# Kernel tuning notes

Hardware: AMD Instinct MI355X
Metric: run time of the kernel (lower is better)

The kernel has to match this reference:

```python
import jax, jax.numpy as jnp
import numpy as np

N = 50000
E = 1600000

def setup_inputs() -> dict:
    key = jax.random.key(0)
    ks = jax.random.split(key, 8)
    x = jax.random.normal(ks[0], (N, 512), dtype=jnp.float32)
    edge_index = jax.random.randint(ks[1], (2, E), 0, N, dtype=jnp.int32).astype(jnp.int64)
    eigenvectors = jax.random.normal(ks[2], (N, 128), dtype=jnp.float32)
    W1 = jax.random.normal(ks[3], (512, 128), dtype=jnp.float32) * 0.04
    b1 = jnp.zeros((128,), dtype=jnp.float32)
    W2 = jax.random.normal(ks[4], (128, 64), dtype=jnp.float32) * 0.09
    b2 = jnp.zeros((64,), dtype=jnp.float32)
    lin_W = jax.random.normal(ks[5], (128, 64), dtype=jnp.float32) * 0.09
    W3 = jax.random.normal(ks[6], (128, 40), dtype=jnp.float32) * 0.09
    b3 = jnp.zeros((40,), dtype=jnp.float32)
    return {"x": x, "edge_index": edge_index, "eigenvectors": eigenvectors,
            "W1": W1, "b1": b1, "W2": W2, "b2": b2, "lin_W": lin_W, "W3": W3, "b3": b3}

def _gcn_norm(edge_index, num_nodes):
    # add self loops, then symmetric normalization D^-1/2 (A+I) D^-1/2
    loop = jnp.arange(num_nodes, dtype=edge_index.dtype)
    row = jnp.concatenate([edge_index[0], loop])  # source
    col = jnp.concatenate([edge_index[1], loop])  # target
    w = jnp.ones(row.shape[0], dtype=jnp.float32)
    deg = jax.ops.segment_sum(w, col, num_segments=num_nodes)
    dis = jnp.where(deg > 0, 1.0 / jnp.sqrt(deg), 0.0)
    norm = dis[row] * dis[col]  # [E+N]
    return row, col, norm

def _gcn_conv(h, W, b, row, col, norm, num_nodes):
    h = h @ W                                  # [N, d_out] linear first (PyG order)
    msg = h[row] * norm[:, None]               # gather + scale, [E+N, d_out]
    out = jax.ops.segment_sum(msg, col, num_segments=num_nodes)  # scatter-add
    return out + b

def reference(x, edge_index, eigenvectors, W1, b1, W2, b2, lin_W, W3, b3):
    num_nodes = x.shape[0]
    row, col, norm = _gcn_norm(edge_index, num_nodes)
    h = jax.nn.relu(_gcn_conv(x, W1, b1, row, col, norm, num_nodes))
    # dropout omitted: eval mode (deterministic reference)
    h = jax.nn.relu(_gcn_conv(h, W2, b2, row, col, norm, num_nodes))
    xp = eigenvectors @ lin_W                  # Linear(spec_in, spec_out, bias=False)
    h = jnp.concatenate([h, xp], axis=1)       # [N, h2+spec_out]
    h = _gcn_conv(h, W3, b3, row, col, norm, num_nodes)
    return jax.nn.log_softmax(h, axis=1)
```

## Files before the change

### kernel.cpp

```cpp
#include <hip/hip_runtime.h>
#include <cstdint>
#include <cstddef>

constexpr int BLK = 256;
constexpr int NB = 128;

static inline size_t ws_align(size_t x) { return (x + 255) & ~size_t(255); }

typedef __attribute__((ext_vector_type(8))) short bf16x8;
typedef __attribute__((ext_vector_type(4))) float f32x4;

__device__ inline unsigned short f2bf(float f) {
  unsigned int u = __float_as_uint(f);
  unsigned int r = (u + 0x7fffu + ((u >> 16) & 1u)) >> 16;
  return (unsigned short)r;
}
__device__ inline float bf2f(unsigned short u) {
  return __uint_as_float(((unsigned int)u) << 16);
}
__device__ inline float bf2f_lo(unsigned int w) {
  return __uint_as_float(w << 16);
}
__device__ inline float bf2f_hi(unsigned int w) {
  return __uint_as_float(w & 0xffff0000u);
}

__device__ inline void gload16(const void* gp, void* lp) {
  __builtin_amdgcn_global_load_lds(
      (const __attribute__((address_space(1))) void*)gp,
      (__attribute__((address_space(3))) void*)lp, 16, 0, 0);
}

__global__ void k_pack_wt(const int* __restrict__ ei, unsigned int* __restrict__ pk,
                          int* __restrict__ cnt, int E, int nChunk,
                          const float* __restrict__ W1, const float* __restrict__ W2,
                          const float* __restrict__ linW, const float* __restrict__ W3,
                          unsigned short* __restrict__ WT1, unsigned short* __restrict__ WT2,
                          unsigned short* __restrict__ WTl, unsigned short* __restrict__ WT3) {
  if (blockIdx.x >= NB) {
    int i = (blockIdx.x - NB) * BLK + threadIdx.x;
    if (i < 65536) {
      int n = i >> 9, k = i & 511;
      WT1[i] = f2bf(W1[(size_t)k * 128 + n]);
    } else if (i < 73728) {
      int j = i - 65536; int n = j >> 7, k = j & 127;
      WT2[j] = f2bf(W2[(size_t)k * 64 + n]);
    } else if (i < 81920) {
      int j = i - 73728; int n = j >> 7, k = j & 127;
      WTl[j] = f2bf(linW[(size_t)k * 64 + n]);
    } else if (i < 88064) {
      int j = i - 81920; int n = j >> 7, k = j & 127;
      WT3[j] = f2bf(n < 40 ? W3[(size_t)k * 40 + n] : 0.f);
    }
    return;
  }
  __shared__ int hist[256];
  for (int t = threadIdx.x; t < 256; t += BLK) hist[t] = 0;
  __syncthreads();
  int allz = 1;
  #pragma unroll 8
  for (int i = 0; i < 32; ++i) allz &= (ei[2 * i + 1] == 0) ? 1 : 0;
  const bool i64 = allz != 0;
  int beg = blockIdx.x * nChunk, end = min(beg + nChunk, E);
  for (int i = beg + threadIdx.x; i < end; i += BLK) {
    int row, col;
    if (i64) { row = ei[2 * i]; col = ei[2 * (E + i)]; }
    else     { row = ei[i];     col = ei[E + i]; }
    unsigned int p = ((unsigned int)col << 16) | (unsigned int)row;
    pk[i] = p;
    atomicAdd(&hist[col >> 8], 1);
  }
  __syncthreads();
  for (int t = threadIdx.x; t < 256; t += BLK) cnt[blockIdx.x * 256 + t] = hist[t];
}

__global__ void k_wscan(const int* __restrict__ cnt, int* __restrict__ woffs,
                        int* __restrict__ base, int nb, int E) {
  __shared__ int wsums[5];
  int w = threadIdx.x;
  int s = 0;
  for (int b = 0; b < nb; ++b) s += cnt[b * 256 + w];
  int lane = w & 63, wv = w >> 6;
  int x = s;
  #pragma unroll
  for (int sh = 1; sh < 64; sh <<= 1) { int t = __shfl_up(x, sh); if (lane >= sh) x += t; }
  if (lane == 63) wsums[wv] = x;
  __syncthreads();
  if (w == 0) { int a = 0; for (int k = 0; k < 4; ++k) { int t = wsums[k]; wsums[k] = a; a += t; } }
  __syncthreads();
  int excl = x - s + wsums[wv];
  woffs[w] = excl;
  if (w == 255) woffs[256] = excl + s;
  int start = excl;
  for (int b = 0; b < nb; ++b) { base[b * 256 + w] = start; start += cnt[b * 256 + w]; }
}

__global__ void k_part_scatter(const unsigned int* __restrict__ pk,
                               const int* __restrict__ base,
                               unsigned int* __restrict__ P, int E, int nChunk) {
  __shared__ int cur[256];
  for (int t = threadIdx.x; t < 256; t += BLK) cur[t] = base[blockIdx.x * 256 + t];
  __syncthreads();
  int beg = blockIdx.x * nChunk, end = min(beg + nChunk, E);
  for (int i = beg + threadIdx.x; i < end; i += BLK) {
    unsigned int p = pk[i];
    int pos = atomicAdd(&cur[p >> 24], 1);
    P[pos] = p;
  }
}

__global__ void k_window_build(const unsigned int* __restrict__ P,
                               const int* __restrict__ woffs,
                               float* __restrict__ dis, int* __restrict__ offs,
                               int* __restrict__ csr, int N, int E) {
  __shared__ int hist[256];
  __shared__ int wsums[5];
  __shared__ int lbase[256];
  const int node0 = blockIdx.x * 256;
  const int t = threadIdx.x;
  hist[t] = 0;
  __syncthreads();
  const int beg = woffs[blockIdx.x], end = woffs[blockIdx.x + 1];
  for (int i = beg + t; i < end; i += BLK)
    atomicAdd(&hist[(P[i] >> 16) & 255], 1);
  __syncthreads();
  const int dg = hist[t];
  if (node0 + t < N) dis[node0 + t] = 1.0f / sqrtf((float)(dg + 1));
  int lane = t & 63, wv = t >> 6;
  int x = dg;
  #pragma unroll
  for (int sh = 1; sh < 64; sh <<= 1) { int q = __shfl_up(x, sh); if (lane >= sh) x += q; }
  if (lane == 63) wsums[wv] = x;
  __syncthreads();
  if (t == 0) { int a = 0; for (int k = 0; k < 4; ++k) { int q = wsums[k]; wsums[k] = a; a += q; } }
  __syncthreads();
  const int goff = beg + (x - dg + wsums[wv]);
  if (node0 + t < N) offs[node0 + t] = goff;
  lbase[t] = goff;
  __syncthreads();
  for (int i = beg + t; i < end; i += BLK) {
    unsigned int p = P[i];
    int pos = atomicAdd(&lbase[(p >> 16) & 255], 1);
    csr[pos] = (int)(p & 0xffffu);
  }
  if (blockIdx.x == 0 && t == 0) offs[N] = E;
}

__global__ __launch_bounds__(256)
void k_gemm1(const float* __restrict__ x, const unsigned short* __restrict__ WT,
             const float* __restrict__ dis, unsigned short* __restrict__ C, int N) {
  __shared__ float As[2][128 * 32];
  __shared__ unsigned short Wsl[2][4 * 128 * 8];
  const int tid = threadIdx.x;
  const int lane = tid & 63, wv = tid >> 6;
  const int m = lane & 15, kq = lane >> 4;
  const int row0 = blockIdx.x * 128;

  const int r8 = lane >> 3;
  const int c8 = lane & 7;
  int agrow[4];
  #pragma unroll
  for (int jj = 0; jj < 4; ++jj) {
    int gr = row0 + wv * 32 + jj * 8 + r8;
    agrow[jj] = gr < N ? gr : N - 1;
  }

  f32x4 acc[2][8];
  #pragma unroll
  for (int mr = 0; mr < 2; ++mr)
    #pragma unroll
    for (int t = 0; t < 8; ++t) acc[mr][t] = {0.f, 0.f, 0.f, 0.f};

  auto STAGE = [&](int pb, int kb) {
    #pragma unroll
    for (int jj = 0; jj < 4; ++jj) {
      const float* src = x + (size_t)agrow[jj] * 512 + kb * 32 + (c8 ^ r8) * 4;
      gload16(src, &As[pb][(wv * 32 + jj * 8) * 32]);
    }
    #pragma unroll
    for (int jj = 0; jj < 2; ++jj) {
      int issue = wv * 2 + jj;
      int slot = issue >> 1, half = issue & 1;
      const unsigned short* src = WT + (size_t)(half * 64 + lane) * 512 + kb * 32 + slot * 8;
      gload16(src, &Wsl[pb][slot * 1024 + half * 512]);
    }
  };

  STAGE(0, 0);
  __syncthreads();

  #pragma unroll 1
  for (int t = 0; t < 16; ++t) {
    const int p = t & 1;
    if (t < 15) STAGE(p ^ 1, t + 1);

    const char* Ab = (const char*)As[p];
    const char* Wb = (const char*)Wsl[p];
    bf16x8 af[2];
    #pragma unroll
    for (int mr = 0; mr < 2; ++mr) {
      int row = wv * 32 + mr * 16 + m;
      int s = row & 7;
      f32x4 lo = *(const f32x4*)(Ab + row * 128 + ((kq * 2) ^ s) * 16);
      f32x4 hi = *(const f32x4*)(Ab + row * 128 + ((kq * 2 + 1) ^ s) * 16);
      af[mr][0] = (short)f2bf(lo[0]); af[mr][1] = (short)f2bf(lo[1]);
      af[mr][2] = (short)f2bf(lo[2]); af[mr][3] = (short)f2bf(lo[3]);
      af[mr][4] = (short)f2bf(hi[0]); af[mr][5] = (short)f2bf(hi[1]);
      af[mr][6] = (short)f2bf(hi[2]); af[mr][7] = (short)f2bf(hi[3]);
    }
    #pragma unroll
    for (int tt = 0; tt < 8; ++tt) {
      bf16x8 bf = *(const bf16x8*)(Wb + kq * 2048 + (tt * 16 + m) * 16);
      #pragma unroll
      for (int mr = 0; mr < 2; ++mr)
        acc[mr][tt] = __builtin_amdgcn_mfma_f32_16x16x32_bf16(af[mr], bf, acc[mr][tt], 0, 0, 0);
    }
    __syncthreads();
  }

  #pragma unroll
  for (int mr = 0; mr < 2; ++mr)
    #pragma unroll
    for (int r = 0; r < 4; ++r) {
      int rr = row0 + wv * 32 + mr * 16 + kq * 4 + r;
      if (rr < N) {
        float s = dis[rr];
        #pragma unroll
        for (int t = 0; t < 8; ++t)
          C[(size_t)rr * 128 + t * 16 + m] = f2bf(acc[mr][t][r] * s);
      }
    }
}

template<int NT, int MR, bool AF32>
__device__ inline void mgemm_body(int bi, const void* __restrict__ Av,
                                  const unsigned short* __restrict__ WT,
                                  const float* __restrict__ dis, unsigned short* __restrict__ C,
                                  int ldc, int NOUT, int N) {
  constexpr int K = 128;
  const int tid = threadIdx.x;
  const int lane = tid & 63;
  const int wv = tid >> 6;
  const int m = lane & 15;
  const int kq = lane >> 4;
  const int orow = bi * (64 * MR) + wv * (16 * MR);

  int rowc[MR];
  #pragma unroll
  for (int mr = 0; mr < MR; ++mr) {
    int row = orow + mr * 16 + m;
    rowc[mr] = row < N ? row : N - 1;
  }

  f32x4 acc[MR][NT];
  #pragma unroll
  for (int mr = 0; mr < MR; ++mr)
    #pragma unroll
    for (int t = 0; t < NT; ++t) acc[mr][t] = {0.f, 0.f, 0.f, 0.f};

  #pragma unroll 4
  for (int k0 = 0; k0 < K; k0 += 32) {
    bf16x8 af[MR];
    #pragma unroll
    for (int mr = 0; mr < MR; ++mr) {
      if constexpr (AF32) {
        const float* Arow = (const float*)Av + (size_t)rowc[mr] * K + kq * 8 + k0;
        float4 a0 = *(const float4*)Arow;
        float4 a1 = *(const float4*)(Arow + 4);
        af[mr][0] = (short)f2bf(a0.x); af[mr][1] = (short)f2bf(a0.y);
        af[mr][2] = (short)f2bf(a0.z); af[mr][3] = (short)f2bf(a0.w);
        af[mr][4] = (short)f2bf(a1.x); af[mr][5] = (short)f2bf(a1.y);
        af[mr][6] = (short)f2bf(a1.z); af[mr][7] = (short)f2bf(a1.w);
      } else {
        const unsigned short* Arow = (const unsigned short*)Av + (size_t)rowc[mr] * K + kq * 8 + k0;
        af[mr] = *(const bf16x8*)Arow;
      }
    }
    bf16x8 bf[NT];
    #pragma unroll
    for (int t = 0; t < NT; ++t)
      bf[t] = *(const bf16x8*)(WT + (size_t)(t * 16 + m) * K + k0 + kq * 8);
    #pragma unroll
    for (int t = 0; t < NT; ++t)
      #pragma unroll
      for (int mr = 0; mr < MR; ++mr)
        acc[mr][t] = __builtin_amdgcn_mfma_f32_16x16x32_bf16(af[mr], bf[t], acc[mr][t], 0, 0, 0);
  }
  #pragma unroll
  for (int mr = 0; mr < MR; ++mr) {
    #pragma unroll
    for (int r = 0; r < 4; ++r) {
      int rr = orow + mr * 16 + kq * 4 + r;
      if (rr < N) {
        float s = dis ? dis[rr] : 1.f;
        #pragma unroll
        for (int t = 0; t < NT; ++t) {
          int cc = t * 16 + m;
          if (cc < NOUT)
            C[(size_t)rr * ldc + cc] = f2bf(acc[mr][t][r] * s);
        }
      }
    }
  }
}

__global__ __launch_bounds__(256)
void k_mgemm2x(const unsigned short* __restrict__ G, const unsigned short* __restrict__ WT2,
               const float* __restrict__ dis, unsigned short* __restrict__ F,
               const float* __restrict__ eig, const unsigned short* __restrict__ WTl,
               unsigned short* __restrict__ XP, int N, int nA) {
  if ((int)blockIdx.x < nA)
    mgemm_body<4, 2, false>(blockIdx.x, G, WT2, dis, F, 64, 64, N);
  else
    mgemm_body<4, 2, true>(blockIdx.x - nA, eig, WTl, nullptr, XP, 64, 64, N);
}

__global__ __launch_bounds__(256)
void k_mgemm3(const unsigned short* __restrict__ H2, const unsigned short* __restrict__ XP,
              const unsigned short* __restrict__ WT3, const float* __restrict__ dis,
              unsigned short* __restrict__ C, int N) {
  constexpr int NT = 3, MR = 2;
  const int tid = threadIdx.x;
  const int lane = tid & 63;
  const int wv = tid >> 6;
  const int m = lane & 15;
  const int kq = lane >> 4;
  const int orow = blockIdx.x * (64 * MR) + wv * (16 * MR);

  int rowc[MR];
  #pragma unroll
  for (int mr = 0; mr < MR; ++mr) {
    int row = orow + mr * 16 + m;
    rowc[mr] = row < N ? row : N - 1;
  }

  f32x4 acc[MR][NT];
  #pragma unroll
  for (int mr = 0; mr < MR; ++mr)
    #pragma unroll
    for (int t = 0; t < NT; ++t) acc[mr][t] = {0.f, 0.f, 0.f, 0.f};

  #pragma unroll 4
  for (int k0 = 0; k0 < 128; k0 += 32) {
    const unsigned short* Abase = (k0 < 64) ? H2 : XP;
    const int kk = (k0 & 63) + kq * 8;
    bf16x8 af[MR];
    #pragma unroll
    for (int mr = 0; mr < MR; ++mr)
      af[mr] = *(const bf16x8*)(Abase + (size_t)rowc[mr] * 64 + kk);
    bf16x8 bf[NT];
    #pragma unroll
    for (int t = 0; t < NT; ++t)
      bf[t] = *(const bf16x8*)(WT3 + (size_t)(t * 16 + m) * 128 + k0 + kq * 8);
    #pragma unroll
    for (int t = 0; t < NT; ++t)
      #pragma unroll
      for (int mr = 0; mr < MR; ++mr)
        acc[mr][t] = __builtin_amdgcn_mfma_f32_16x16x32_bf16(af[mr], bf[t], acc[mr][t], 0, 0, 0);
  }
  #pragma unroll
  for (int mr = 0; mr < MR; ++mr) {
    #pragma unroll
    for (int r = 0; r < 4; ++r) {
      int rr = orow + mr * 16 + kq * 4 + r;
      if (rr < N) {
        float s = dis[rr];
        #pragma unroll
        for (int t = 0; t < NT; ++t) {
          int cc = t * 16 + m;
          if (cc < 40)
            C[(size_t)rr * 40 + cc] = f2bf(acc[mr][t][r] * s);
        }
      }
    }
  }
}

template<int D, bool RELU>
__launch_bounds__(BLK)
__global__ void k_agg2(const unsigned short* __restrict__ g, int ldg,
                       const float* __restrict__ dis, const float* __restrict__ bias,
                       const int* __restrict__ offs, const int* __restrict__ csr,
                       unsigned short* __restrict__ dst, int ldd, int N) {
  constexpr int CPL = D / 32;
  int wid = (blockIdx.x * BLK + threadIdx.x) >> 6;
  int lane = threadIdx.x & 63;
  if (wid >= N) return;
  const int l5 = lane >> 5, c = lane & 31;
  float acc[CPL];
  #pragma unroll
  for (int k = 0; k < CPL; ++k) acc[k] = 0.f;

  auto addrow = [&](int r) {
    if constexpr (CPL == 4) {
      uint2 w = *(const uint2*)&g[(size_t)r * ldg + c * 4];
      acc[0] += bf2f_lo(w.x); acc[1] += bf2f_hi(w.x);
      acc[2] += bf2f_lo(w.y); acc[3] += bf2f_hi(w.y);
    } else {
      unsigned int w = *(const unsigned int*)&g[(size_t)r * ldg + c * 2];
      acc[0] += bf2f_lo(w); acc[1] += bf2f_hi(w);
    }
  };

  if (l5 == 0) addrow(wid);
  int beg = offs[wid], end = offs[wid + 1];
  for (int e0 = beg; e0 < end; e0 += 64) {
    int cnt = end - e0; if (cnt > 64) cnt = 64;
    int u = (lane < cnt) ? csr[e0 + lane] : 0;
    int j = 0;
    for (; j + 3 < cnt; j += 4) {
      int r0 = __shfl(u, j + l5);
      int r1 = __shfl(u, j + 2 + l5);
      addrow(r0); addrow(r1);
    }
    for (; j < cnt; j += 2) {
      int jj = j + l5;
      int r0 = __shfl(u, jj < cnt ? jj : j);
      if (jj < cnt) addrow(r0);
    }
  }
  #pragma unroll
  for (int k = 0; k < CPL; ++k) acc[k] += __shfl_xor(acc[k], 32);

  if (l5 == 0) {
    float dv = dis[wid];
    float o[CPL];
    #pragma unroll
    for (int k = 0; k < CPL; ++k) {
      o[k] = dv * acc[k] + bias[c * CPL + k];
      if constexpr (RELU) o[k] = fmaxf(o[k], 0.f);
    }
    if constexpr (CPL == 4) {
      uint2 pw;
      pw.x = (unsigned)f2bf(o[0]) | ((unsigned)f2bf(o[1]) << 16);
      pw.y = (unsigned)f2bf(o[2]) | ((unsigned)f2bf(o[3]) << 16);
      *(uint2*)&dst[(size_t)wid * ldd + c * 4] = pw;
    } else {
      unsigned int pw = (unsigned)f2bf(o[0]) | ((unsigned)f2bf(o[1]) << 16);
      *(unsigned int*)&dst[(size_t)wid * ldd + c * 2] = pw;
    }
  }
}

__launch_bounds__(BLK)
__global__ void k_agg40(const unsigned short* __restrict__ g,
                        const float* __restrict__ dis, const float* __restrict__ bias,
                        const int* __restrict__ offs, const int* __restrict__ csr,
                        float* __restrict__ dst, int N) {
  int wid = (blockIdx.x * BLK + threadIdx.x) >> 6;
  int lane = threadIdx.x & 63;
  if (wid >= N) return;
  const int l5 = lane >> 5, c = lane & 31;
  const bool act = c < 20;
  float a0 = 0.f, a1 = 0.f;
  auto addrow = [&](int r) {
    if (act) {
      unsigned int w = *(const unsigned int*)&g[(size_t)r * 40 + c * 2];
      a0 += bf2f_lo(w); a1 += bf2f_hi(w);
    }
  };
  if (l5 == 0) addrow(wid);
  int beg = offs[wid], end = offs[wid + 1];
  for (int e0 = beg; e0 < end; e0 += 64) {
    int cnt = end - e0; if (cnt > 64) cnt = 64;
    int u = (lane < cnt) ? csr[e0 + lane] : 0;
    int j = 0;
    for (; j + 3 < cnt; j += 4) {
      int r0 = __shfl(u, j + l5);
      int r1 = __shfl(u, j + 2 + l5);
      addrow(r0); addrow(r1);
    }
    for (; j < cnt; j += 2) {
      int jj = j + l5;
      int r0 = __shfl(u, jj < cnt ? jj : j);
      if (jj < cnt) addrow(r0);
    }
  }
  a0 += __shfl_xor(a0, 32);
  a1 += __shfl_xor(a1, 32);

  if (l5 == 0) {
    float dv = dis[wid];
    float o0 = act ? dv * a0 + bias[c * 2]     : -__builtin_inff();
    float o1 = act ? dv * a1 + bias[c * 2 + 1] : -__builtin_inff();
    float mx = fmaxf(o0, o1);
    #pragma unroll
    for (int s = 16; s >= 1; s >>= 1) mx = fmaxf(mx, __shfl_down(mx, s, 32));
    mx = __shfl(mx, 0, 32);
    float ex = act ? (expf(o0 - mx) + expf(o1 - mx)) : 0.f;
    #pragma unroll
    for (int s = 16; s >= 1; s >>= 1) ex += __shfl_down(ex, s, 32);
    float ls = logf(__shfl(ex, 0, 32));
    if (act) {
      float2 r = make_float2(o0 - mx - ls, o1 - mx - ls);
      *(float2*)&dst[(size_t)wid * 40 + c * 2] = r;
    }
  }
}

extern "C" void kernel_launch(void* const* d_in, const int* in_sizes, int n_in,
                              void* d_out, int out_size, void* d_ws, size_t ws_size,
                              hipStream_t stream) {
  const float* x    = (const float*)d_in[0];
  const int*   ei   = (const int*)d_in[1];
  const float* eig  = (const float*)d_in[2];
  const float* W1   = (const float*)d_in[3];
  const float* b1   = (const float*)d_in[4];
  const float* W2   = (const float*)d_in[5];
  const float* b2   = (const float*)d_in[6];
  const float* linW = (const float*)d_in[7];
  const float* W3   = (const float*)d_in[8];
  const float* b3   = (const float*)d_in[9];
  float* out = (float*)d_out;

  const int N = in_sizes[0] / 512;
  const int E = in_sizes[1] / 2;

  char* ws = (char*)d_ws;
  size_t off = 0;
  auto alloc = [&](size_t bytes) { char* p = ws + off; off = ws_align(off + bytes); return p; };
  unsigned int* pk = (unsigned int*)alloc((size_t)E * 4);
  unsigned int* P  = (unsigned int*)alloc((size_t)E * 4);
  int*   csr    = (int*)alloc((size_t)E * 4);
  int*   offs   = (int*)alloc((size_t)(N + 1) * 4);
  int*   cnt    = (int*)alloc((size_t)NB * 256 * 4);
  int*   base   = (int*)alloc((size_t)NB * 256 * 4);
  int*   woffs  = (int*)alloc(257 * 4);
  float* dis    = (float*)alloc((size_t)N * 4);
  unsigned short* F  = (unsigned short*)alloc((size_t)N * 128 * 2);
  unsigned short* G  = (unsigned short*)alloc((size_t)N * 128 * 2);
  unsigned short* XP = (unsigned short*)alloc((size_t)N * 64 * 2);
  unsigned short* H2 = (unsigned short*)alloc((size_t)N * 64 * 2);
  unsigned short* WT1 = (unsigned short*)alloc(128 * 512 * 2);
  unsigned short* WT2 = (unsigned short*)alloc(64 * 128 * 2);
  unsigned short* WTl = (unsigned short*)alloc(64 * 128 * 2);
  unsigned short* WT3 = (unsigned short*)alloc(48 * 128 * 2);

  const int nChunk = (E + NB - 1) / NB;
  const int NW = (N + 255) / 256;
  const int WTB = (88064 + BLK - 1) / BLK;

  k_pack_wt<<<NB + WTB, BLK, 0, stream>>>(ei, pk, cnt, E, nChunk,
                                          W1, W2, linW, W3, WT1, WT2, WTl, WT3);
  k_wscan<<<1, 256, 0, stream>>>(cnt, woffs, base, NB, E);
  k_part_scatter<<<NB, BLK, 0, stream>>>(pk, base, P, E, nChunk);
  k_window_build<<<NW, BLK, 0, stream>>>(P, woffs, dis, offs, csr, N, E);

  const int gG1 = (N + 127) / 128;
  const int gA = (N + 3) / 4;

  k_gemm1<<<gG1, BLK, 0, stream>>>(x, WT1, dis, F, N);
  k_agg2<128, true><<<gA, BLK, 0, stream>>>(F, 128, dis, b1, offs, csr, G, 128, N);
  k_mgemm2x<<<2 * gG1, BLK, 0, stream>>>(G, WT2, dis, F, eig, WTl, XP, N, gG1);
  k_agg2<64, true><<<gA, BLK, 0, stream>>>(F, 64, dis, b2, offs, csr, H2, 64, N);
  k_mgemm3<<<gG1, BLK, 0, stream>>>(H2, XP, WT3, dis, F, N);
  k_agg40<<<gA, BLK, 0, stream>>>(F, dis, b3, offs, csr, out, N);
}
```

Before: 293.4 us.

## Merge edge partition scatter with layer-1 GEMM and move dis scaling into aggregation

The edge partition scatter and the first x@W1 GEMM now run as one launch, with disjoint block ranges doing each job. This lets the GEMM run concurrently with the graph preprocessing instead of waiting for dis. Because dis is not ready yet, the GEMM no longer scales rows by dis. The first aggregation now gathers dis[u] per neighbour and applies it with an FMA, which adds a gathered load and shuffles per edge. The combined kernel uses a 48KB shared buffer for both roles, which may lower occupancy for the scatter blocks.

```diff
diff --git a/kernel.cpp b/kernel.cpp
--- a/kernel.cpp
+++ b/kernel.cpp
@@ -95,18 +95,104 @@
   for (int b = 0; b < nb; ++b) { base[b * 256 + w] = start; start += cnt[b * 256 + w]; }
 }
 
-__global__ void k_part_scatter(const unsigned int* __restrict__ pk,
-                               const int* __restrict__ base,
-                               unsigned int* __restrict__ P, int E, int nChunk) {
-  __shared__ int cur[256];
-  for (int t = threadIdx.x; t < 256; t += BLK) cur[t] = base[blockIdx.x * 256 + t];
-  __syncthreads();
-  int beg = blockIdx.x * nChunk, end = min(beg + nChunk, E);
-  for (int i = beg + threadIdx.x; i < end; i += BLK) {
-    unsigned int p = pk[i];
-    int pos = atomicAdd(&cur[p >> 24], 1);
-    P[pos] = p;
-  }
+__global__ __launch_bounds__(256)
+void k_part_gemm1(const unsigned int* __restrict__ pk, const int* __restrict__ base,
+                  unsigned int* __restrict__ P, int E, int nChunk,
+                  const float* __restrict__ x, const unsigned short* __restrict__ WT,
+                  unsigned short* __restrict__ C, int N) {
+  __shared__ __align__(16) char smem[49152];
+  if (blockIdx.x < NB) {
+    int* cur = (int*)smem;
+    for (int t = threadIdx.x; t < 256; t += BLK) cur[t] = base[blockIdx.x * 256 + t];
+    __syncthreads();
+    int beg = blockIdx.x * nChunk, end = min(beg + nChunk, E);
+    for (int i = beg + threadIdx.x; i < end; i += BLK) {
+      unsigned int p = pk[i];
+      int pos = atomicAdd(&cur[p >> 24], 1);
+      P[pos] = p;
+    }
+    return;
+  }
+  float* As0 = (float*)smem;
+  unsigned short* Wsl0 = (unsigned short*)(smem + 32768);
+  const int tid = threadIdx.x;
+  const int lane = tid & 63, wv = tid >> 6;
+  const int m = lane & 15, kq = lane >> 4;
+  const int row0 = ((int)blockIdx.x - NB) * 128;
+
+  const int r8 = lane >> 3;
+  const int c8 = lane & 7;
+  int agrow[4];
+  #pragma unroll
+  for (int jj = 0; jj < 4; ++jj) {
+    int gr = row0 + wv * 32 + jj * 8 + r8;
+    agrow[jj] = gr < N ? gr : N - 1;
+  }
+
+  f32x4 acc[2][8];
+  #pragma unroll
+  for (int mr = 0; mr < 2; ++mr)
+    #pragma unroll
+    for (int t = 0; t < 8; ++t) acc[mr][t] = {0.f, 0.f, 0.f, 0.f};
+
+  auto STAGE = [&](int pb, int kb) {
+    #pragma unroll
+    for (int jj = 0; jj < 4; ++jj) {
+      const float* src = x + (size_t)agrow[jj] * 512 + kb * 32 + (c8 ^ r8) * 4;
+      gload16(src, As0 + pb * 4096 + (wv * 32 + jj * 8) * 32);
+    }
+    #pragma unroll
+    for (int jj = 0; jj < 2; ++jj) {
+      int issue = wv * 2 + jj;
+      int slot = issue >> 1, half = issue & 1;
+      const unsigned short* src = WT + (size_t)(half * 64 + lane) * 512 + kb * 32 + slot * 8;
+      gload16(src, Wsl0 + pb * 4096 + slot * 1024 + half * 512);
+    }
+  };
+
+  STAGE(0, 0);
+  __syncthreads();
+
+  #pragma unroll 1
+  for (int t = 0; t < 16; ++t) {
+    const int p = t & 1;
+    if (t < 15) STAGE(p ^ 1, t + 1);
+
+    const char* Ab = (const char*)(As0 + p * 4096);
+    const char* Wb = (const char*)(Wsl0 + p * 4096);
+    bf16x8 af[2];
+    #pragma unroll
+    for (int mr = 0; mr < 2; ++mr) {
+      int row = wv * 32 + mr * 16 + m;
+      int s = row & 7;
+      f32x4 lo = *(const f32x4*)(Ab + row * 128 + ((kq * 2) ^ s) * 16);
+      f32x4 hi = *(const f32x4*)(Ab + row * 128 + ((kq * 2 + 1) ^ s) * 16);
+      af[mr][0] = (short)f2bf(lo[0]); af[mr][1] = (short)f2bf(lo[1]);
+      af[mr][2] = (short)f2bf(lo[2]); af[mr][3] = (short)f2bf(lo[3]);
+      af[mr][4] = (short)f2bf(hi[0]); af[mr][5] = (short)f2bf(hi[1]);
+      af[mr][6] = (short)f2bf(hi[2]); af[mr][7] = (short)f2bf(hi[3]);
+    }
+    #pragma unroll
+    for (int tt = 0; tt < 8; ++tt) {
+      bf16x8 bf = *(const bf16x8*)(Wb + kq * 2048 + (tt * 16 + m) * 16);
+      #pragma unroll
+      for (int mr = 0; mr < 2; ++mr)
+        acc[mr][tt] = __builtin_amdgcn_mfma_f32_16x16x32_bf16(af[mr], bf, acc[mr][tt], 0, 0, 0);
+    }
+    __syncthreads();
+  }
+
+  #pragma unroll
+  for (int mr = 0; mr < 2; ++mr)
+    #pragma unroll
+    for (int r = 0; r < 4; ++r) {
+      int rr = row0 + wv * 32 + mr * 16 + kq * 4 + r;
+      if (rr < N) {
+        #pragma unroll
+        for (int t = 0; t < 8; ++t)
+          C[(size_t)rr * 128 + t * 16 + m] = f2bf(acc[mr][t][r]);
+      }
+    }
 }
 
 __global__ void k_window_build(const unsigned int* __restrict__ P,
@@ -144,92 +230,6 @@
     csr[pos] = (int)(p & 0xffffu);
   }
   if (blockIdx.x == 0 && t == 0) offs[N] = E;
-}
-
-__global__ __launch_bounds__(256)
-void k_gemm1(const float* __restrict__ x, const unsigned short* __restrict__ WT,
-             const float* __restrict__ dis, unsigned short* __restrict__ C, int N) {
-  __shared__ float As[2][128 * 32];
-  __shared__ unsigned short Wsl[2][4 * 128 * 8];
-  const int tid = threadIdx.x;
-  const int lane = tid & 63, wv = tid >> 6;
-  const int m = lane & 15, kq = lane >> 4;
-  const int row0 = blockIdx.x * 128;
-
-  const int r8 = lane >> 3;
-  const int c8 = lane & 7;
-  int agrow[4];
-  #pragma unroll
-  for (int jj = 0; jj < 4; ++jj) {
-    int gr = row0 + wv * 32 + jj * 8 + r8;
-    agrow[jj] = gr < N ? gr : N - 1;
-  }
-
-  f32x4 acc[2][8];
-  #pragma unroll
-  for (int mr = 0; mr < 2; ++mr)
-    #pragma unroll
-    for (int t = 0; t < 8; ++t) acc[mr][t] = {0.f, 0.f, 0.f, 0.f};
-
-  auto STAGE = [&](int pb, int kb) {
-    #pragma unroll
-    for (int jj = 0; jj < 4; ++jj) {
-      const float* src = x + (size_t)agrow[jj] * 512 + kb * 32 + (c8 ^ r8) * 4;
-      gload16(src, &As[pb][(wv * 32 + jj * 8) * 32]);
-    }
-    #pragma unroll
-    for (int jj = 0; jj < 2; ++jj) {
-      int issue = wv * 2 + jj;
-      int slot = issue >> 1, half = issue & 1;
-      const unsigned short* src = WT + (size_t)(half * 64 + lane) * 512 + kb * 32 + slot * 8;
-      gload16(src, &Wsl[pb][slot * 1024 + half * 512]);
-    }
-  };
-
-  STAGE(0, 0);
-  __syncthreads();
-
-  #pragma unroll 1
-  for (int t = 0; t < 16; ++t) {
-    const int p = t & 1;
-    if (t < 15) STAGE(p ^ 1, t + 1);
-
-    const char* Ab = (const char*)As[p];
-    const char* Wb = (const char*)Wsl[p];
-    bf16x8 af[2];
-    #pragma unroll
-    for (int mr = 0; mr < 2; ++mr) {
-      int row = wv * 32 + mr * 16 + m;
-      int s = row & 7;
-      f32x4 lo = *(const f32x4*)(Ab + row * 128 + ((kq * 2) ^ s) * 16);
-      f32x4 hi = *(const f32x4*)(Ab + row * 128 + ((kq * 2 + 1) ^ s) * 16);
-      af[mr][0] = (short)f2bf(lo[0]); af[mr][1] = (short)f2bf(lo[1]);
-      af[mr][2] = (short)f2bf(lo[2]); af[mr][3] = (short)f2bf(lo[3]);
-      af[mr][4] = (short)f2bf(hi[0]); af[mr][5] = (short)f2bf(hi[1]);
-      af[mr][6] = (short)f2bf(hi[2]); af[mr][7] = (short)f2bf(hi[3]);
-    }
-    #pragma unroll
-    for (int tt = 0; tt < 8; ++tt) {
-      bf16x8 bf = *(const bf16x8*)(Wb + kq * 2048 + (tt * 16 + m) * 16);
-      #pragma unroll
-      for (int mr = 0; mr < 2; ++mr)
-        acc[mr][tt] = __builtin_amdgcn_mfma_f32_16x16x32_bf16(af[mr], bf, acc[mr][tt], 0, 0, 0);
-    }
-    __syncthreads();
-  }
-
-  #pragma unroll
-  for (int mr = 0; mr < 2; ++mr)
-    #pragma unroll
-    for (int r = 0; r < 4; ++r) {
-      int rr = row0 + wv * 32 + mr * 16 + kq * 4 + r;
-      if (rr < N) {
-        float s = dis[rr];
-        #pragma unroll
-        for (int t = 0; t < 8; ++t)
-          C[(size_t)rr * 128 + t * 16 + m] = f2bf(acc[mr][t][r] * s);
-      }
-    }
 }
 
 template<int NT, int MR, bool AF32>
@@ -376,7 +376,7 @@
   }
 }
 
-template<int D, bool RELU>
+template<int D, bool RELU, bool GDIS>
 __launch_bounds__(BLK)
 __global__ void k_agg2(const unsigned short* __restrict__ g, int ldg,
                        const float* __restrict__ dis, const float* __restrict__ bias,
@@ -387,43 +387,49 @@
   int lane = threadIdx.x & 63;
   if (wid >= N) return;
   const int l5 = lane >> 5, c = lane & 31;
+  const float dv = dis[wid];
   float acc[CPL];
   #pragma unroll
   for (int k = 0; k < CPL; ++k) acc[k] = 0.f;
 
-  auto addrow = [&](int r) {
+  auto addrow = [&](int r, float w) {
     if constexpr (CPL == 4) {
-      uint2 w = *(const uint2*)&g[(size_t)r * ldg + c * 4];
-      acc[0] += bf2f_lo(w.x); acc[1] += bf2f_hi(w.x);
-      acc[2] += bf2f_lo(w.y); acc[3] += bf2f_hi(w.y);
+      uint2 v = *(const uint2*)&g[(size_t)r * ldg + c * 4];
+      acc[0] = fmaf(w, bf2f_lo(v.x), acc[0]); acc[1] = fmaf(w, bf2f_hi(v.x), acc[1]);
+      acc[2] = fmaf(w, bf2f_lo(v.y), acc[2]); acc[3] = fmaf(w, bf2f_hi(v.y), acc[3]);
     } else {
-      unsigned int w = *(const unsigned int*)&g[(size_t)r * ldg + c * 2];
-      acc[0] += bf2f_lo(w); acc[1] += bf2f_hi(w);
+      unsigned int v = *(const unsigned int*)&g[(size_t)r * ldg + c * 2];
+      acc[0] = fmaf(w, bf2f_lo(v), acc[0]); acc[1] = fmaf(w, bf2f_hi(v), acc[1]);
     }
   };
 
-  if (l5 == 0) addrow(wid);
+  if (l5 == 0) addrow(wid, GDIS ? dv : 1.0f);
   int beg = offs[wid], end = offs[wid + 1];
   for (int e0 = beg; e0 < end; e0 += 64) {
     int cnt = end - e0; if (cnt > 64) cnt = 64;
     int u = (lane < cnt) ? csr[e0 + lane] : 0;
+    float du = 1.0f;
+    if constexpr (GDIS) du = (lane < cnt) ? dis[u] : 0.f;
     int j = 0;
     for (; j + 3 < cnt; j += 4) {
       int r0 = __shfl(u, j + l5);
       int r1 = __shfl(u, j + 2 + l5);
-      addrow(r0); addrow(r1);
+      float w0 = GDIS ? __shfl(du, j + l5) : 1.0f;
+      float w1 = GDIS ? __shfl(du, j + 2 + l5) : 1.0f;
+      addrow(r0, w0); addrow(r1, w1);
     }
     for (; j < cnt; j += 2) {
       int jj = j + l5;
-      int r0 = __shfl(u, jj < cnt ? jj : j);
-      if (jj < cnt) addrow(r0);
+      int si = jj < cnt ? jj : j;
+      int r0 = __shfl(u, si);
+      float w0 = GDIS ? __shfl(du, si) : 1.0f;
+      if (jj < cnt) addrow(r0, w0);
     }
   }
   #pragma unroll
   for (int k = 0; k < CPL; ++k) acc[k] += __shfl_xor(acc[k], 32);
 
   if (l5 == 0) {
-    float dv = dis[wid];
     float o[CPL];
     #pragma unroll
     for (int k = 0; k < CPL; ++k) {
@@ -539,20 +545,18 @@
   const int nChunk = (E + NB - 1) / NB;
   const int NW = (N + 255) / 256;
   const int WTB = (88064 + BLK - 1) / BLK;
+  const int gG1 = (N + 127) / 128;
+  const int gA = (N + 3) / 4;
 
   k_pack_wt<<<NB + WTB, BLK, 0, stream>>>(ei, pk, cnt, E, nChunk,
                                           W1, W2, linW, W3, WT1, WT2, WTl, WT3);
   k_wscan<<<1, 256, 0, stream>>>(cnt, woffs, base, NB, E);
-  k_part_scatter<<<NB, BLK, 0, stream>>>(pk, base, P, E, nChunk);
+  k_part_gemm1<<<NB + gG1, BLK, 0, stream>>>(pk, base, P, E, nChunk, x, WT1, F, N);
   k_window_build<<<NW, BLK, 0, stream>>>(P, woffs, dis, offs, csr, N, E);
 
-  const int gG1 = (N + 127) / 128;
-  const int gA = (N + 3) / 4;
-
-  k_gemm1<<<gG1, BLK, 0, stream>>>(x, WT1, dis, F, N);
-  k_agg2<128, true><<<gA, BLK, 0, stream>>>(F, 128, dis, b1, offs, csr, G, 128, N);
+  k_agg2<128, true, true><<<gA, BLK, 0, stream>>>(F, 128, dis, b1, offs, csr, G, 128, N);
   k_mgemm2x<<<2 * gG1, BLK, 0, stream>>>(G, WT2, dis, F, eig, WTl, XP, N, gG1);
-  k_agg2<64, true><<<gA, BLK, 0, stream>>>(F, 64, dis, b2, offs, csr, H2, 64, N);
+  k_agg2<64, true, false><<<gA, BLK, 0, stream>>>(F, 64, dis, b2, offs, csr, H2, 64, N);
   k_mgemm3<<<gG1, BLK, 0, stream>>>(H2, XP, WT3, dis, F, N);
   k_agg40<<<gA, BLK, 0, stream>>>(F, dis, b3, offs, csr, out, N);
 }
```

Measured after the change: 286.0 us. 1.03x faster.
